# Kernel optimization log

Measured on AMD Instinct MI355X. Metric: run time of the kernel, lower is better.

Reference implementation:

```python
import jax, jax.numpy as jnp
import numpy as np

B, T, H, F = 128, 512, 1024, 1  # batch, num_steps, rnn_hidden_dim, num_features


def setup_inputs() -> dict:
    key = jax.random.key(0)
    ks = jax.random.split(key, 12)
    s = 1.0 / np.sqrt(H)  # PyTorch LSTM default init scale
    inp = {
        "sequence": jax.random.normal(ks[0], (B, T, F), dtype=jnp.float32),
        "z": jax.random.normal(ks[1], (B, H), dtype=jnp.float32),
        # layer 0: input size F=1
        "W_ih0": jax.random.uniform(ks[2], (4 * H, F), minval=-s, maxval=s),
        "W_hh0": jax.random.uniform(ks[3], (4 * H, H), minval=-s, maxval=s),
        "b_ih0": jax.random.uniform(ks[4], (4 * H,), minval=-s, maxval=s),
        "b_hh0": jax.random.uniform(ks[5], (4 * H,), minval=-s, maxval=s),
        # layer 1: input size H
        "W_ih1": jax.random.uniform(ks[6], (4 * H, H), minval=-s, maxval=s),
        "W_hh1": jax.random.uniform(ks[7], (4 * H, H), minval=-s, maxval=s),
        "b_ih1": jax.random.uniform(ks[8], (4 * H,), minval=-s, maxval=s),
        "b_hh1": jax.random.uniform(ks[9], (4 * H,), minval=-s, maxval=s),
        # output projection Linear(H, F)
        "W_out": jax.random.uniform(ks[10], (F, H), minval=-s, maxval=s),
        "b_out": jnp.full((F,), 0.01, dtype=jnp.float32),
    }
    return inp


def _lstm_cell(x, h, c, W_ih, W_hh, b_ih, b_hh):
    # PyTorch gate order: i, f, g, o
    g = x @ W_ih.T + h @ W_hh.T + (b_ih + b_hh)  # [B, 4H]
    i, f, gg, o = jnp.split(g, 4, axis=-1)
    i, f, o = jax.nn.sigmoid(i), jax.nn.sigmoid(f), jax.nn.sigmoid(o)
    c_new = f * c + i * jnp.tanh(gg)
    h_new = o * jnp.tanh(c_new)
    return h_new, c_new


def reference(sequence, z, W_ih0, W_hh0, b_ih0, b_hh0,
              W_ih1, W_hh1, b_ih1, b_hh1, W_out, b_out):
    batch = sequence.shape[0]
    # hidden = (z.repeat(num_layers,1,1), z.repeat(num_layers,1,1)) -> both
    # layers initialized with z for h and c.
    init = (z, z, z, z, jnp.zeros((batch, F), dtype=sequence.dtype))

    def step(carry, _):
        h0, c0, h1, c1, pred = carry
        h0, c0 = _lstm_cell(pred, h0, c0, W_ih0, W_hh0, b_ih0, b_hh0)
        h1, c1 = _lstm_cell(h0, h1, c1, W_ih1, W_hh1, b_ih1, b_hh1)
        pred = h1 @ W_out.T + b_out  # [B, 1]
        return (h0, c0, h1, c1, pred), pred

    _, preds = jax.lax.scan(step, init, None, length=sequence.shape[1])
    recovered = jnp.transpose(preds, (1, 0, 2))  # [B, T, 1]
    loss = jnp.mean((sequence - recovered) ** 2)  # MSE criterion
    return loss, recovered
```

## Files before the change

kernel.cpp:

```cpp
#include <hip/hip_runtime.h>
#include <hip/hip_bf16.h>

#define HID 1024
#define BATCH 128
#define TSTEPS 512
#define NWG 256
#define NTHR 512

typedef __bf16 bf16x4 __attribute__((ext_vector_type(4)));
typedef __bf16 bf16x8 __attribute__((ext_vector_type(8)));
typedef float f32x4 __attribute__((ext_vector_type(4)));

#define ASTORE_U(p,v) __hip_atomic_store((p),(v),__ATOMIC_RELAXED,__HIP_MEMORY_SCOPE_AGENT)
#define ASTORE_F(p,v) __hip_atomic_store((p),(v),__ATOMIC_RELAXED,__HIP_MEMORY_SCOPE_AGENT)
#define ALOAD_U(p)    __hip_atomic_load((p),__ATOMIC_RELAXED,__HIP_MEMORY_SCOPE_AGENT)
#define ALOAD_F(p)    __hip_atomic_load((p),__ATOMIC_RELAXED,__HIP_MEMORY_SCOPE_AGENT)
#define ALOAD_ULL(p)  __hip_atomic_load((p),__ATOMIC_RELAXED,__HIP_MEMORY_SCOPE_AGENT)
#define AADD_U(p,v)   __hip_atomic_fetch_add((p),(v),__ATOMIC_RELAXED,__HIP_MEMORY_SCOPE_AGENT)

__device__ __forceinline__ float sigm(float x){ return 1.f/(1.f+__expf(-x)); }

__device__ __forceinline__ bf16x8 cvt8(const float* __restrict__ p){
  bf16x8 r;
  #pragma unroll
  for (int i=0;i<8;i++) r[i] = (__bf16)p[i];
  return r;
}
__device__ __forceinline__ bf16x8 cvt8s(const float* __restrict__ p, float s){
  bf16x8 r;
  #pragma unroll
  for (int i=0;i<8;i++) r[i] = (__bf16)(p[i]*s);
  return r;
}

__global__ void init_kernel(const float* __restrict__ z,
                            unsigned short* __restrict__ st0,
                            unsigned* __restrict__ bar){
  int i = blockIdx.x*blockDim.x + threadIdx.x;
  if (i < 1024) bar[i] = 0u;
  for (int idx = i; idx < BATCH*HID; idx += 65536){
    int blk = idx >> 9, rem = idx & 511, b = rem >> 2, du = rem & 3;
    st0[idx] = __builtin_bit_cast(unsigned short, (__bf16)z[b*HID + blk*4 + du]);
  }
}

#define GRP_CTR(g)  ((g)*32)
#define MID_CTR     256
#define GRP_FLAG(g) (320 + (g)*32)

__global__ __launch_bounds__(NTHR, 2) void lstm_kernel(
    const float* __restrict__ seq,
    const float* __restrict__ z,
    const float* __restrict__ Wih0, const float* __restrict__ Whh0,
    const float* __restrict__ bih0, const float* __restrict__ bhh0,
    const float* __restrict__ Wih1, const float* __restrict__ Whh1,
    const float* __restrict__ bih1, const float* __restrict__ bhh1,
    const float* __restrict__ Wout, const float* __restrict__ bout,
    float* __restrict__ out,
    unsigned short* __restrict__ st0,
    unsigned short* __restrict__ st1,
    float* __restrict__ predpart,
    float* __restrict__ shalf,
    float* __restrict__ losspart,
    unsigned* __restrict__ bar)
{
  const int tid  = threadIdx.x;
  const int wg   = blockIdx.x;
  const int wid  = tid >> 6;
  const int lane = tid & 63;
  const int u0   = wg << 2;

  __shared__ bf16x8 wlds[4][32][64];
  __shared__ float finals2[16*132];
  __shared__ float pr2[2];
  __shared__ float sb0p[16], sb0f[16], sb1[16];

  const float bout_s = bout[0];

  if (tid < 16) {
    int g = tid >> 2, du = tid & 3;
    int gc = g*HID + u0 + du;
    float bp = bih0[gc] + bhh0[gc];
    sb0p[tid] = bp;
    sb0f[tid] = bp + Wih0[gc]*bout_s;
    sb1[tid]  = bih1[gc] + bhh1[gc];
  }

  const int eb  = tid >> 2;
  const int edu = tid & 3;
  const float wout_u = Wout[u0 + edu];
  float c0 = z[eb*HID + u0 + edu];
  float c1 = c0;
  float lossacc = 0.f;
  float myhalf  = 0.f;

  const int bcol = lane & 15;
  const int gcol = (bcol >> 2)*HID + u0 + (bcol & 3);
  const int ksub = (lane >> 4) << 3;
  {
    const float wih0c = Wih0[gcol];
    #pragma unroll
    for (int ktl=0; ktl<4; ++ktl) {
      int k0  = (wid << 7) + (ktl << 5) + ksub;
      int ktg = (wid << 2) + ktl;
      wlds[0][ktg][lane] = cvt8(Whh0 + gcol*HID + k0);
      wlds[1][ktg][lane] = cvt8(Wih1 + gcol*HID + k0);
      wlds[2][ktg][lane] = cvt8(Whh1 + gcol*HID + k0);
      wlds[3][ktg][lane] = cvt8s(Wout + k0, wih0c);
    }
  }
  __syncthreads();

  f32x4 accG0{0,0,0,0}, accG1{0,0,0,0};
  unsigned gen = 0;

  const int hi2 = (lane >> 4) << 1;
  const int bb4 = ((wid << 4) + (lane & 15)) << 2;

  auto ldfrag = [&](const unsigned short* __restrict__ src, int kt)->bf16x8{
    const unsigned short* p = src + (size_t)(((kt << 3) + hi2) * 512) + bb4;
    unsigned long long lo64 = ALOAD_ULL((const unsigned long long*)p);
    unsigned long long hi64 = ALOAD_ULL((const unsigned long long*)(p + 512));
    bf16x4 lo = __builtin_bit_cast(bf16x4, lo64);
    bf16x4 hi = __builtin_bit_cast(bf16x4, hi64);
    return __builtin_shufflevector(lo, hi, 0,1,2,3,4,5,6,7);
  };

  auto do_pass = [&](const unsigned short* __restrict__ src, int matA, int matB,
                     f32x4& accA, f32x4& accB){
    bf16x8 af[8];
    #pragma unroll
    for (int i=0;i<8;i++) af[i] = ldfrag(src, i);
    #pragma unroll
    for (int kt=0; kt<32; ++kt){
      bf16x8 a = af[kt & 7];
      accA = __builtin_amdgcn_mfma_f32_16x16x32_bf16(a, wlds[matA][kt][lane], accA, 0, 0, 0);
      accB = __builtin_amdgcn_mfma_f32_16x16x32_bf16(a, wlds[matB][kt][lane], accB, 0, 0, 0);
      if (kt < 24) af[kt & 7] = ldfrag(src, kt + 8);
    }
  };

  auto publish = [&](f32x4& acc, const float* sbias){
    float bias = sbias[lane & 15];
    int base = (lane & 15)*132 + (wid << 4) + ((lane >> 4) << 2);
    #pragma unroll
    for (int e=0;e<4;e++) finals2[base + e] = acc[e] + bias;
    __syncthreads();
    acc = f32x4{0,0,0,0};
  };

  auto elementwise = [&](float& c, unsigned short* __restrict__ stdst, bool dopred){
    float gi = finals2[(edu   )*132 + eb];
    float gf = finals2[(edu+ 4)*132 + eb];
    float gg = finals2[(edu+ 8)*132 + eb];
    float go = finals2[(edu+12)*132 + eb];
    float fi = sigm(gi), ff = sigm(gf), fo = sigm(go);
    c = ff*c + fi*tanhf(gg);
    float h = fo*tanhf(c);
    unsigned h16 = (unsigned)__builtin_bit_cast(unsigned short, (__bf16)h);
    unsigned other = (unsigned)__shfl_xor((int)h16, 1);
    if (!(tid & 1)) {
      unsigned word = h16 | (other << 16);
      ASTORE_U((unsigned*)(stdst + wg*512 + tid), word);
    }
    if (dopred){
      float pv = h * wout_u;
      pv += __shfl_xor(pv, 1);
      pv += __shfl_xor(pv, 2);
      if (edu == 0) ASTORE_F(&predpart[wg*128 + eb], pv);
    }
  };

  auto grid_barrier = [&](){
    __syncthreads();
    ++gen;
    if (tid == 0) {
      unsigned old = AADD_U(&bar[GRP_CTR(wg & 7)], 1u);
      if (old == gen*32u - 1u) {
        unsigned r = AADD_U(&bar[MID_CTR], 1u);
        if (r == gen*8u - 1u) {
          #pragma unroll
          for (int g2=0; g2<8; ++g2) ASTORE_U(&bar[GRP_FLAG(g2)], gen);
        }
      }
      while (ALOAD_U(&bar[GRP_FLAG(wg & 7)]) < gen)
        __builtin_amdgcn_s_sleep(4);
    }
    __syncthreads();
  };

  do_pass(st0, 0, 2, accG0, accG1);
  grid_barrier();
  publish(accG0, sb0p);
  elementwise(c0, st0, false);
  grid_barrier();

  for (int t=0; t<TSTEPS; ++t) {
    do_pass(st0, 1, 0, accG1, accG0);
    float oh = 0.f;
    if (t > 0 && wg < BATCH && tid == 0) oh = ALOAD_F(&shalf[wg]);
    publish(accG1, sb1);
    if (t > 0 && wg < BATCH && tid == 0) {
      float pred = myhalf + oh + bout_s;
      out[1 + wg*TSTEPS + (t-1)] = pred;
      float d = seq[wg*TSTEPS + (t-1)] - pred;
      lossacc += d*d;
    }
    elementwise(c1, st1, true);
    grid_barrier();

    float hred = 0.f;
    if (tid < 128)
      hred = ALOAD_F(&predpart[((wg >> 7)*128 + tid)*128 + (wg & 127)]);
    do_pass(st1, 3, 2, accG0, accG1);
    hred += __shfl_xor(hred, 1);  hred += __shfl_xor(hred, 2);
    hred += __shfl_xor(hred, 4);  hred += __shfl_xor(hred, 8);
    hred += __shfl_xor(hred, 16); hred += __shfl_xor(hred, 32);
    if (tid == 0)  pr2[0] = hred;
    if (tid == 64) pr2[1] = hred;
    publish(accG0, sb0f);
    if (tid == 0) {
      float hs = pr2[0] + pr2[1];
      if (wg >= BATCH) ASTORE_F(&shalf[wg - BATCH], hs);
      else             myhalf = hs;
    }
    elementwise(c0, st0, false);
    grid_barrier();
  }

  if (wg < BATCH && tid == 0) {
    float oh2 = ALOAD_F(&shalf[wg]);
    float pred = myhalf + oh2 + bout_s;
    out[1 + wg*TSTEPS + (TSTEPS-1)] = pred;
    float d = seq[wg*TSTEPS + (TSTEPS-1)] - pred;
    lossacc += d*d;
    ASTORE_F(&losspart[wg], lossacc);
  }
  grid_barrier();
  if (wg == 0) {
    float v = 0.f;
    if (tid < BATCH) v = ALOAD_F(&losspart[tid]);
    v += __shfl_xor(v, 1);  v += __shfl_xor(v, 2);
    v += __shfl_xor(v, 4);  v += __shfl_xor(v, 8);
    v += __shfl_xor(v, 16); v += __shfl_xor(v, 32);
    if (tid == 0)  pr2[0] = v;
    if (tid == 64) pr2[1] = v;
    __syncthreads();
    if (tid == 0) out[0] = (pr2[0] + pr2[1]) * (1.f/65536.f);
  }
}

extern "C" void kernel_launch(void* const* d_in, const int* in_sizes, int n_in,
                              void* d_out, int out_size, void* d_ws, size_t ws_size,
                              hipStream_t stream)
{
  const float* seq  = (const float*)d_in[0];
  const float* z    = (const float*)d_in[1];
  const float* Wih0 = (const float*)d_in[2];
  const float* Whh0 = (const float*)d_in[3];
  const float* bih0 = (const float*)d_in[4];
  const float* bhh0 = (const float*)d_in[5];
  const float* Wih1 = (const float*)d_in[6];
  const float* Whh1 = (const float*)d_in[7];
  const float* bih1 = (const float*)d_in[8];
  const float* bhh1 = (const float*)d_in[9];
  const float* Wout = (const float*)d_in[10];
  const float* bout = (const float*)d_in[11];
  float* out = (float*)d_out;

  char* ws = (char*)d_ws;
  unsigned short* st0 = (unsigned short*)(ws);
  unsigned short* st1 = (unsigned short*)(ws + 256*1024);
  unsigned* bar   = (unsigned*)(ws + 512*1024);
  float* predpart = (float*)(ws + 516*1024);
  float* shalf    = (float*)(ws + 644*1024);
  float* losspart = (float*)(ws + 644*1024 + 512);

  hipLaunchKernelGGL(init_kernel, dim3(256), dim3(256), 0, stream, z, st0, bar);

  void* args[] = { (void*)&seq, (void*)&z, (void*)&Wih0, (void*)&Whh0, (void*)&bih0, (void*)&bhh0,
                   (void*)&Wih1, (void*)&Whh1, (void*)&bih1, (void*)&bhh1, (void*)&Wout, (void*)&bout,
                   (void*)&out, (void*)&st0, (void*)&st1, (void*)&predpart, (void*)&shalf,
                   (void*)&losspart, (void*)&bar };
  hipLaunchCooperativeKernel((void*)lstm_kernel, dim3(NWG), dim3(NTHR), args, 0u, stream);
}
```

Before: 6.436 ms.

## Exchange hidden state between workgroups as int8 instead of bf16

Result: no change. 6.494 ms (+0.9%).

```diff
diff --git a/kernel.cpp b/kernel.cpp
--- a/kernel.cpp
+++ b/kernel.cpp
@@ -20,12 +20,6 @@
 
 __device__ __forceinline__ float sigm(float x){ return 1.f/(1.f+__expf(-x)); }
 
-__device__ __forceinline__ bf16x8 cvt8(const float* __restrict__ p){
-  bf16x8 r;
-  #pragma unroll
-  for (int i=0;i<8;i++) r[i] = (__bf16)p[i];
-  return r;
-}
 __device__ __forceinline__ bf16x8 cvt8s(const float* __restrict__ p, float s){
   bf16x8 r;
   #pragma unroll
@@ -34,13 +28,14 @@
 }
 
 __global__ void init_kernel(const float* __restrict__ z,
-                            unsigned short* __restrict__ st0,
+                            unsigned short* __restrict__ zst,
                             unsigned* __restrict__ bar){
   int i = blockIdx.x*blockDim.x + threadIdx.x;
   if (i < 1024) bar[i] = 0u;
   for (int idx = i; idx < BATCH*HID; idx += 65536){
     int blk = idx >> 9, rem = idx & 511, b = rem >> 2, du = rem & 3;
-    st0[idx] = __builtin_bit_cast(unsigned short, (__bf16)z[b*HID + blk*4 + du]);
+    zst[idx] = __builtin_bit_cast(unsigned short,
+                 (__bf16)(z[b*HID + blk*4 + du] * 127.f));
   }
 }
 
@@ -57,8 +52,9 @@
     const float* __restrict__ bih1, const float* __restrict__ bhh1,
     const float* __restrict__ Wout, const float* __restrict__ bout,
     float* __restrict__ out,
-    unsigned short* __restrict__ st0,
-    unsigned short* __restrict__ st1,
+    unsigned char* __restrict__ st0q,
+    unsigned char* __restrict__ st1q,
+    const unsigned short* __restrict__ zst,
     float* __restrict__ predpart,
     float* __restrict__ shalf,
     float* __restrict__ losspart,
@@ -76,6 +72,7 @@
   __shared__ float sb0p[16], sb0f[16], sb1[16];
 
   const float bout_s = bout[0];
+  const float ISC = 1.f/127.f;
 
   if (tid < 16) {
     int g = tid >> 2, du = tid & 3;
@@ -103,10 +100,10 @@
     for (int ktl=0; ktl<4; ++ktl) {
       int k0  = (wid << 7) + (ktl << 5) + ksub;
       int ktg = (wid << 2) + ktl;
-      wlds[0][ktg][lane] = cvt8(Whh0 + gcol*HID + k0);
-      wlds[1][ktg][lane] = cvt8(Wih1 + gcol*HID + k0);
-      wlds[2][ktg][lane] = cvt8(Whh1 + gcol*HID + k0);
-      wlds[3][ktg][lane] = cvt8s(Wout + k0, wih0c);
+      wlds[0][ktg][lane] = cvt8s(Whh0 + gcol*HID + k0, ISC);
+      wlds[1][ktg][lane] = cvt8s(Wih1 + gcol*HID + k0, ISC);
+      wlds[2][ktg][lane] = cvt8s(Whh1 + gcol*HID + k0, ISC);
+      wlds[3][ktg][lane] = cvt8s(Wout + k0, wih0c * ISC);
     }
   }
   __syncthreads();
@@ -117,8 +114,8 @@
   const int hi2 = (lane >> 4) << 1;
   const int bb4 = ((wid << 4) + (lane & 15)) << 2;
 
-  auto ldfrag = [&](const unsigned short* __restrict__ src, int kt)->bf16x8{
-    const unsigned short* p = src + (size_t)(((kt << 3) + hi2) * 512) + bb4;
+  auto ldfragz = [&](int kt)->bf16x8{
+    const unsigned short* p = zst + (size_t)(((kt << 3) + hi2) * 512) + bb4;
     unsigned long long lo64 = ALOAD_ULL((const unsigned long long*)p);
     unsigned long long hi64 = ALOAD_ULL((const unsigned long long*)(p + 512));
     bf16x4 lo = __builtin_bit_cast(bf16x4, lo64);
@@ -126,17 +123,44 @@
     return __builtin_shufflevector(lo, hi, 0,1,2,3,4,5,6,7);
   };
 
-  auto do_pass = [&](const unsigned short* __restrict__ src, int matA, int matB,
-                     f32x4& accA, f32x4& accB){
-    bf16x8 af[8];
-    #pragma unroll
-    for (int i=0;i<8;i++) af[i] = ldfrag(src, i);
+  auto ld_i8 = [&](const unsigned char* __restrict__ src, int kt,
+                   unsigned& lo, unsigned& hi){
+    const unsigned char* p = src + (size_t)(((kt << 3) + hi2) * 512) + bb4;
+    lo = ALOAD_U((const unsigned*)p);
+    hi = ALOAD_U((const unsigned*)(p + 512));
+  };
+  auto dq8 = [&](unsigned lo, unsigned hi)->bf16x8{
+    bf16x8 r;
+    #pragma unroll
+    for (int i=0;i<4;i++){
+      int q0 = (int)(lo << (24 - 8*i)) >> 24;
+      int q1 = (int)(hi << (24 - 8*i)) >> 24;
+      r[i]   = (__bf16)(float)q0;
+      r[4+i] = (__bf16)(float)q1;
+    }
+    return r;
+  };
+
+  auto do_pass_pro = [&](int matA, int matB, f32x4& accA, f32x4& accB){
     #pragma unroll
     for (int kt=0; kt<32; ++kt){
-      bf16x8 a = af[kt & 7];
+      bf16x8 a = ldfragz(kt);
       accA = __builtin_amdgcn_mfma_f32_16x16x32_bf16(a, wlds[matA][kt][lane], accA, 0, 0, 0);
       accB = __builtin_amdgcn_mfma_f32_16x16x32_bf16(a, wlds[matB][kt][lane], accB, 0, 0, 0);
-      if (kt < 24) af[kt & 7] = ldfrag(src, kt + 8);
+    }
+  };
+
+  auto do_pass = [&](const unsigned char* __restrict__ src, int matA, int matB,
+                     f32x4& accA, f32x4& accB){
+    unsigned rl[8], rh[8];
+    #pragma unroll
+    for (int i=0;i<8;i++) ld_i8(src, i, rl[i], rh[i]);
+    #pragma unroll
+    for (int kt=0; kt<32; ++kt){
+      bf16x8 a = dq8(rl[kt & 7], rh[kt & 7]);
+      accA = __builtin_amdgcn_mfma_f32_16x16x32_bf16(a, wlds[matA][kt][lane], accA, 0, 0, 0);
+      accB = __builtin_amdgcn_mfma_f32_16x16x32_bf16(a, wlds[matB][kt][lane], accB, 0, 0, 0);
+      if (kt < 24) ld_i8(src, kt + 8, rl[kt & 7], rh[kt & 7]);
     }
   };
 
@@ -149,7 +173,7 @@
     acc = f32x4{0,0,0,0};
   };
 
-  auto elementwise = [&](float& c, unsigned short* __restrict__ stdst, bool dopred){
+  auto elementwise = [&](float& c, unsigned char* __restrict__ stdst, bool dopred){
     float gi = finals2[(edu   )*132 + eb];
     float gf = finals2[(edu+ 4)*132 + eb];
     float gg = finals2[(edu+ 8)*132 + eb];
@@ -157,12 +181,12 @@
     float fi = sigm(gi), ff = sigm(gf), fo = sigm(go);
     c = ff*c + fi*tanhf(gg);
     float h = fo*tanhf(c);
-    unsigned h16 = (unsigned)__builtin_bit_cast(unsigned short, (__bf16)h);
-    unsigned other = (unsigned)__shfl_xor((int)h16, 1);
-    if (!(tid & 1)) {
-      unsigned word = h16 | (other << 16);
-      ASTORE_U((unsigned*)(stdst + wg*512 + tid), word);
-    }
+    int q = (int)__builtin_rintf(h * 127.f);
+    unsigned b8 = ((unsigned)q & 0xFFu) << (edu*8);
+    b8 |= (unsigned)__shfl_xor((int)b8, 1);
+    b8 |= (unsigned)__shfl_xor((int)b8, 2);
+    if (edu == 0)
+      ASTORE_U((unsigned*)(stdst + wg*512 + (eb << 2)), b8);
     if (dopred){
       float pv = h * wout_u;
       pv += __shfl_xor(pv, 1);
@@ -189,14 +213,14 @@
     __syncthreads();
   };
 
-  do_pass(st0, 0, 2, accG0, accG1);
+  do_pass_pro(0, 2, accG0, accG1);
   grid_barrier();
   publish(accG0, sb0p);
-  elementwise(c0, st0, false);
+  elementwise(c0, st0q, false);
   grid_barrier();
 
   for (int t=0; t<TSTEPS; ++t) {
-    do_pass(st0, 1, 0, accG1, accG0);
+    do_pass(st0q, 1, 0, accG1, accG0);
     float oh = 0.f;
     if (t > 0 && wg < BATCH && tid == 0) oh = ALOAD_F(&shalf[wg]);
     publish(accG1, sb1);
@@ -206,13 +230,13 @@
       float d = seq[wg*TSTEPS + (t-1)] - pred;
       lossacc += d*d;
     }
-    elementwise(c1, st1, true);
+    elementwise(c1, st1q, true);
     grid_barrier();
 
     float hred = 0.f;
     if (tid < 128)
       hred = ALOAD_F(&predpart[((wg >> 7)*128 + tid)*128 + (wg & 127)]);
-    do_pass(st1, 3, 2, accG0, accG1);
+    do_pass(st1q, 3, 2, accG0, accG1);
     hred += __shfl_xor(hred, 1);  hred += __shfl_xor(hred, 2);
     hred += __shfl_xor(hred, 4);  hred += __shfl_xor(hred, 8);
     hred += __shfl_xor(hred, 16); hred += __shfl_xor(hred, 32);
@@ -224,7 +248,7 @@
       if (wg >= BATCH) ASTORE_F(&shalf[wg - BATCH], hs);
       else             myhalf = hs;
     }
-    elementwise(c0, st0, false);
+    elementwise(c0, st0q, false);
     grid_barrier();
   }
 
@@ -269,18 +293,19 @@
   float* out = (float*)d_out;
 
   char* ws = (char*)d_ws;
-  unsigned short* st0 = (unsigned short*)(ws);
-  unsigned short* st1 = (unsigned short*)(ws + 256*1024);
+  unsigned char*  st0q = (unsigned char*)(ws);
+  unsigned char*  st1q = (unsigned char*)(ws + 128*1024);
+  unsigned short* zst  = (unsigned short*)(ws + 256*1024);
   unsigned* bar   = (unsigned*)(ws + 512*1024);
   float* predpart = (float*)(ws + 516*1024);
   float* shalf    = (float*)(ws + 644*1024);
   float* losspart = (float*)(ws + 644*1024 + 512);
 
-  hipLaunchKernelGGL(init_kernel, dim3(256), dim3(256), 0, stream, z, st0, bar);
+  hipLaunchKernelGGL(init_kernel, dim3(256), dim3(256), 0, stream, z, zst, bar);
 
   void* args[] = { (void*)&seq, (void*)&z, (void*)&Wih0, (void*)&Whh0, (void*)&bih0, (void*)&bhh0,
                    (void*)&Wih1, (void*)&Whh1, (void*)&bih1, (void*)&bhh1, (void*)&Wout, (void*)&bout,
-                   (void*)&out, (void*)&st0, (void*)&st1, (void*)&predpart, (void*)&shalf,
-                   (void*)&losspart, (void*)&bar };
+                   (void*)&out, (void*)&st0q, (void*)&st1q, (void*)&zst, (void*)&predpart,
+                   (void*)&shalf, (void*)&losspart, (void*)&bar };
   hipLaunchCooperativeKernel((void*)lstm_kernel, dim3(NWG), dim3(NTHR), args, 0u, stream);
 }
```
